# Kernel tuning notes

Hardware: AMD Instinct MI355X
Metric: run time of the kernel (lower is better)

The kernel has to match this reference:

```python
import jax, jax.numpy as jnp
import numpy as np

S, B, C, H, W = 3, 4, 256, 64, 64
NH, HD = 8, 32  # heads, head_dim (C = NH*HD)
EPS = 1e-5  # BatchNorm eps (torch default)


def _bn_params(k, n, c):
    k1, k2, k3, k4 = jax.random.split(k, 4)
    gamma = 1.0 + 0.1 * jax.random.normal(k1, (n, c))
    beta = 0.1 * jax.random.normal(k2, (n, c))
    mean = 0.1 * jax.random.normal(k3, (n, c))
    var = jax.random.uniform(k4, (n, c), minval=0.5, maxval=1.5)
    return jnp.stack([gamma, beta, mean, var], axis=1).astype(jnp.float32)  # [n,4,c]


def setup_inputs() -> dict:
    key = jax.random.key(0)
    ks = jax.random.split(key, 20)
    rn = lambda k, sh, s=0.02: (s * jax.random.normal(k, sh)).astype(jnp.float32)
    inp = {
        'x': jax.random.normal(ks[0], (S, B, C, H, W), jnp.float32),
        'Wq': rn(ks[1], (S, C, C)), 'bq': rn(ks[2], (S, C)), 'bn_q': _bn_params(ks[3], S, C),
        'Wk': rn(ks[4], (S, C, C)), 'bk': rn(ks[5], (S, C)), 'bn_k': _bn_params(ks[6], S, C),
        'Wv': rn(ks[7], (S, C, C)), 'bv': rn(ks[8], (S, C)), 'bn_v': _bn_params(ks[9], S, C),
        'imp_w1': rn(ks[10], (C, S * C)), 'imp_b1': rn(ks[10], (C,)),
        'imp_w2': rn(ks[11], (S, C)), 'imp_b2': rn(ks[11], (S,)),
        'attn_in_w': rn(ks[12], (3 * C, C)), 'attn_in_b': rn(ks[13], (3 * C,)),
        'attn_out_w': rn(ks[14], (C, C)), 'attn_out_b': rn(ks[15], (C,)),
        'op_w1': rn(ks[16], (C, C, 3, 3)), 'op_b1': rn(ks[17], (C,)),
        'op_bn': _bn_params(ks[18], 1, C)[0],  # [4,C]
        'op_w2': rn(ks[19], (C, C)), 'op_b2': rn(ks[19], (C,)),
        'target_h': H, 'target_w': W,
    }
    return inp


def _proj(x, Wt, bt, bnt):
    # per-scale 1x1 conv + BatchNorm (inference) + exact GELU; x:[S,B,C,H,W]
    y = jnp.einsum('sbchw,soc->sbohw', x, Wt) + bt[:, None, :, None, None]
    g, be, mu, var = bnt[:, 0], bnt[:, 1], bnt[:, 2], bnt[:, 3]
    sc = g * jax.lax.rsqrt(var + EPS)
    y = (y - mu[:, None, :, None, None]) * sc[:, None, :, None, None] + be[:, None, :, None, None]
    return jax.nn.gelu(y, approximate=False)


def _bn1(y, bn):  # y:[B,C,H,W], bn:[4,C]
    g, be, mu, var = bn[0], bn[1], bn[2], bn[3]
    sc = g * jax.lax.rsqrt(var + EPS)
    return (y - mu[None, :, None, None]) * sc[None, :, None, None] + be[None, :, None, None]


def _forward(x, Wq, bq, bn_q, Wk, bk, bn_k, Wv, bv, bn_v,
             imp_w1, imp_b1, imp_w2, imp_b2,
             attn_in_w, attn_in_b, attn_out_w, attn_out_b,
             op_w1, op_b1, op_bn, op_w2, op_b2):
    # scale-importance weights from global pooled concat [B, S*C]
    pooled = x.mean(axis=(3, 4)).transpose(1, 0, 2).reshape(B, S * C)
    h = jax.nn.gelu(pooled @ imp_w1.T + imp_b1, approximate=False)
    w = jax.nn.softmax(h @ imp_w2.T + imp_b2, axis=1)  # [B,S]

    q = _proj(x, Wq, bq, bn_q)
    k = _proj(x, Wk, bk, bn_k)
    v = _proj(x, Wv, bv, bn_v)

    N = B * H * W
    tok = lambda t: t.transpose(1, 3, 4, 0, 2).reshape(N, S, C)  # [N,S,C]
    Wiq, Wik, Wiv = attn_in_w[:C], attn_in_w[C:2 * C], attn_in_w[2 * C:]
    biq, bik, biv = attn_in_b[:C], attn_in_b[C:2 * C], attn_in_b[2 * C:]
    qt = (tok(q) @ Wiq.T + biq).reshape(N, S, NH, HD).transpose(0, 2, 1, 3)
    kt = (tok(k) @ Wik.T + bik).reshape(N, S, NH, HD).transpose(0, 2, 1, 3)
    vt = (tok(v) @ Wiv.T + biv).reshape(N, S, NH, HD).transpose(0, 2, 1, 3)
    scores = jnp.einsum('nhsd,nhtd->nhst', qt, kt) / jnp.sqrt(jnp.float32(HD))
    attn = jax.nn.softmax(scores, axis=-1)  # dropout=0.1 is inactive in eval
    o = jnp.einsum('nhst,nhtd->nhsd', attn, vt).transpose(0, 2, 1, 3).reshape(N, S, C)
    o = o @ attn_out_w.T + attn_out_b
    attn_sp = o.reshape(B, H, W, S, C).transpose(3, 0, 4, 1, 2)  # [S,B,C,H,W]

    integrated = jnp.einsum('sbchw,bs->bchw', attn_sp, w)

    y = jax.lax.conv_general_dilated(integrated, op_w1, (1, 1), 'SAME',
                                     dimension_numbers=('NCHW', 'OIHW', 'NCHW'))
    y = y + op_b1[None, :, None, None]
    y = jax.nn.gelu(_bn1(y, op_bn), approximate=False)
    y = jnp.einsum('bchw,oc->bohw', y, op_w2) + op_b2[None, :, None, None]
    return y + x[1]  # residual with second (resized) scale


def reference(x, Wq, bq, bn_q, Wk, bk, bn_k, Wv, bv, bn_v,
              imp_w1, imp_b1, imp_w2, imp_b2,
              attn_in_w, attn_in_b, attn_out_w, attn_out_b,
              op_w1, op_b1, op_bn, op_w2, op_b2, target_h, target_w):
    return _forward(x, Wq, bq, bn_q, Wk, bk, bn_k, Wv, bv, bn_v,
                    imp_w1, imp_b1, imp_w2, imp_b2,
                    attn_in_w, attn_in_b, attn_out_w, attn_out_b,
                    op_w1, op_b1, op_bn, op_w2, op_b2)
```

## Files before the change

### kernel.cpp

```cpp
#include <hip/hip_runtime.h>
#include <hip/hip_bf16.h>
#include <math.h>

#define S_ 3
#define B_ 4
#define C_ 256
#define H_ 64
#define W_ 64
#define HW_ 4096
#define CHW_ (C_*HW_)
#define NH_ 8
#define HD_ 32
#define EPS_ 1e-5f

typedef float  f32x4 __attribute__((ext_vector_type(4)));
typedef short  s16x8 __attribute__((ext_vector_type(8)));
typedef unsigned short u16x4 __attribute__((ext_vector_type(4)));
typedef unsigned int   u32x2 __attribute__((ext_vector_type(2)));
typedef int    s32x4 __attribute__((ext_vector_type(4)));

static constexpr size_t HALFB  = (size_t)S_*B_*CHW_*2;
static constexpr size_t QB     = (size_t)B_*CHW_*2;
static constexpr size_t O_XB   = 0;
static constexpr size_t O_S0B  = HALFB;
static constexpr size_t O_BUFA = 2*HALFB;
static constexpr size_t O_BUFB = 3*HALFB;
static constexpr size_t O_OMB  = 4*HALFB;
static constexpr size_t O_INTB = 4*HALFB + QB;
static constexpr size_t O_CVB  = 4*HALFB + 2*QB;
static constexpr size_t O_AW   = 4*HALFB + 3*QB;
static constexpr size_t O_WB   = O_AW + (size_t)B_*NH_*3*HW_*4;
static constexpr size_t WB_ELEMS = 1507328;
static constexpr size_t O_POOL = O_WB + WB_ELEMS*2;
static constexpr size_t O_H    = O_POOL + (size_t)B_*S_*C_*4;
static constexpr size_t O_WSM  = O_H + (size_t)B_*C_*4;
static constexpr size_t WO_WQ  = 0;
static constexpr size_t WO_WK  = 196608;
static constexpr size_t WO_WV  = 393216;
static constexpr size_t WO_AIW = 589824;
static constexpr size_t WO_AOW = 786432;
static constexpr size_t WO_CW  = 851968;
static constexpr size_t WO_FW2 = 1441792;

__device__ __forceinline__ float gelu_exact(float x) {
    return 0.5f * x * (1.0f + erff(x * 0.70710678118654752440f));
}
__device__ __forceinline__ unsigned short f2bf(float f) {
    union { float f; unsigned u; } x; x.f = f;
    unsigned r = x.u + 0x7FFFu + ((x.u >> 16) & 1u);
    return (unsigned short)(r >> 16);
}
__device__ __forceinline__ float bf2f(unsigned short h) {
    union { unsigned u; float f; } x; x.u = ((unsigned)h) << 16;
    return x.f;
}

__global__ __launch_bounds__(256)
void cast_w(const float* __restrict__ w0, const float* __restrict__ w1,
            const float* __restrict__ w2, const float* __restrict__ w3,
            const float* __restrict__ w4, const float* __restrict__ w5,
            const float* __restrict__ w6, unsigned short* __restrict__ dst) {
    int blk = blockIdx.x;
    const float* src; size_t base;
    if      (blk < 48)  { src = w0; base = WO_WQ;  }
    else if (blk < 96)  { src = w1; base = WO_WK;  blk -= 48; }
    else if (blk < 144) { src = w2; base = WO_WV;  blk -= 96; }
    else if (blk < 192) { src = w3; base = WO_AIW; blk -= 144; }
    else if (blk < 208) { src = w4; base = WO_AOW; blk -= 192; }
    else if (blk < 352) { src = w5; base = WO_CW;  blk -= 208; }
    else                { src = w6; base = WO_FW2; blk -= 352; }
    size_t off = (size_t)blk*4096 + threadIdx.x*4;
    #pragma unroll
    for (int it = 0; it < 4; ++it, off += 1024) {
        float4 v = *(const float4*)&src[off];
        u16x4 h; h[0] = f2bf(v.x); h[1] = f2bf(v.y); h[2] = f2bf(v.z); h[3] = f2bf(v.w);
        *(u16x4*)&dst[base + off] = h;
    }
}

__global__ __launch_bounds__(256)
void cast_pool(const float* __restrict__ x, unsigned short* __restrict__ xb,
               float* __restrict__ pooled) {
    const int blk = blockIdx.x;
    const int c  = blk & (C_-1);
    const int sb = blk >> 8;
    const int s  = sb >> 2, b = sb & 3;
    const float* p = x + (size_t)blk * HW_;
    unsigned short* q = xb + (size_t)blk * HW_;
    float sum = 0.f;
    int i = threadIdx.x * 4;
    #pragma unroll
    for (int it = 0; it < 4; ++it, i += 1024) {
        float4 v = *(const float4*)&p[i];
        sum += v.x + v.y + v.z + v.w;
        u16x4 h; h[0] = f2bf(v.x); h[1] = f2bf(v.y); h[2] = f2bf(v.z); h[3] = f2bf(v.w);
        *(u16x4*)&q[i] = h;
    }
    #pragma unroll
    for (int off = 32; off; off >>= 1) sum += __shfl_down(sum, off);
    __shared__ float red[4];
    if ((threadIdx.x & 63) == 0) red[threadIdx.x >> 6] = sum;
    __syncthreads();
    if (threadIdx.x == 0) {
        float t = red[0] + red[1] + red[2] + red[3];
        pooled[b * (S_*C_) + s * C_ + c] = t * (1.0f / HW_);
    }
}

__global__ __launch_bounds__(256)
void imp1(const float* __restrict__ pooled, const float* __restrict__ w1,
          const float* __restrict__ b1, float* __restrict__ h) {
    const int o = blockIdx.x;
    const int tid = threadIdx.x;
    float part[4] = {0.f, 0.f, 0.f, 0.f};
    for (int j = tid; j < S_*C_; j += 256) {
        const float wv = w1[o * (S_*C_) + j];
        #pragma unroll
        for (int b = 0; b < 4; ++b) part[b] = fmaf(pooled[b*(S_*C_) + j], wv, part[b]);
    }
    #pragma unroll
    for (int off = 32; off; off >>= 1)
        #pragma unroll
        for (int b = 0; b < 4; ++b) part[b] += __shfl_down(part[b], off);
    __shared__ float red[4][4];
    if ((tid & 63) == 0) {
        #pragma unroll
        for (int b = 0; b < 4; ++b) red[tid >> 6][b] = part[b];
    }
    __syncthreads();
    if (tid < 4) {
        float t = red[0][tid] + red[1][tid] + red[2][tid] + red[3][tid];
        h[tid * C_ + o] = gelu_exact(t + b1[o]);
    }
}

__global__ __launch_bounds__(256)
void imp2(const float* __restrict__ h, const float* __restrict__ w2,
          const float* __restrict__ b2, float* __restrict__ wout) {
    __shared__ float hl[B_*C_];
    __shared__ float lg[4][3];
    const int tid = threadIdx.x;
    for (int i = tid; i < B_*C_; i += 256) hl[i] = h[i];
    __syncthreads();
    if (tid < 12) {
        const int b = tid / 3, s = tid % 3;
        float a = b2[s];
        for (int o = 0; o < C_; ++o) a = fmaf(hl[b*C_ + o], w2[s*C_ + o], a);
        lg[b][s] = a;
    }
    __syncthreads();
    if (tid < 4) {
        const float m = fmaxf(fmaxf(lg[tid][0], lg[tid][1]), lg[tid][2]);
        const float e0 = expf(lg[tid][0]-m), e1 = expf(lg[tid][1]-m), e2 = expf(lg[tid][2]-m);
        const float inv = 1.0f / (e0 + e1 + e2);
        wout[tid*3+0] = e0*inv; wout[tid*3+1] = e1*inv; wout[tid*3+2] = e2*inv;
    }
}

template<int MODE>
__global__ __launch_bounds__(256)
void mgemm(const unsigned short* __restrict__ In, const unsigned short* __restrict__ Wb,
           const float* __restrict__ bias, const float* __restrict__ bnp,
           const float* __restrict__ resid, void* __restrict__ Out, int perS) {
    __shared__ __align__(16) unsigned short Ash[4096];
    __shared__ __align__(16) unsigned short Bsh[4096];
    __shared__ float2 ep[128];

    const int z    = blockIdx.z;
    const int widx = perS ? (z >> 2) : 0;
    const unsigned short* Wm = Wb + (size_t)widx * (C_*C_);
    const unsigned short* in = In + (size_t)z * CHW_;
    const int tid  = threadIdx.x;
    const int lane = tid & 63;
    const int wid  = tid >> 6;
    const int nBase = blockIdx.x * 128;
    const int mBase = blockIdx.y * 128;
    const int wm = (wid >> 1) * 64;
    const int wn = (wid & 1) * 64;

    if (tid < 128) {
        const int o = mBase + tid;
        float mulc = 1.f, addc = bias[widx*C_ + o];
        if constexpr (MODE == 0) {
            const float g  = bnp[(size_t)widx*4*C_ + o];
            const float be = bnp[(size_t)widx*4*C_ + C_   + o];
            const float mu = bnp[(size_t)widx*4*C_ + 2*C_ + o];
            const float va = bnp[(size_t)widx*4*C_ + 3*C_ + o];
            mulc = g * rsqrtf(va + EPS_);
            addc = (addc - mu) * mulc + be;
        }
        ep[tid] = make_float2(mulc, addc);
    }

    const f32x4 zero = {0.f, 0.f, 0.f, 0.f};
    f32x4 acc[4][4];
    #pragma unroll
    for (int i = 0; i < 4; ++i)
        #pragma unroll
        for (int j = 0; j < 4; ++j) acc[i][j] = zero;

    for (int k0 = 0; k0 < C_; k0 += 32) {
        __syncthreads();
        #pragma unroll
        for (int it = 0; it < 4; ++it) {
            const int idx = tid + it*256;
            const int m = idx >> 3, q = idx & 7;
            u16x4 v = *(const u16x4*)&Wm[(size_t)(mBase + m)*C_ + k0 + 4*q];
            u32x2 w; w[0] = (unsigned)v[0] | ((unsigned)v[1] << 16);
                     w[1] = (unsigned)v[2] | ((unsigned)v[3] << 16);
            *(u32x2*)((char*)Ash + ((m>>4)*1024 + ((m&15) + 16*(q>>1))*16 + (q&1)*8)) = w;
        }
        #pragma unroll
        for (int it = 0; it < 4; ++it) {
            const int idx = tid + it*256;
            const int n = idx & 127, kq = idx >> 7;
            const size_t gb = (size_t)(k0 + 4*kq)*HW_ + nBase + n;
            unsigned short e0 = in[gb], e1 = in[gb + HW_], e2 = in[gb + 2*HW_], e3 = in[gb + 3*HW_];
            u32x2 w; w[0] = (unsigned)e0 | ((unsigned)e1 << 16);
                     w[1] = (unsigned)e2 | ((unsigned)e3 << 16);
            *(u32x2*)((char*)Bsh + ((n>>4)*1024 + ((n&15) + 16*(kq>>1))*16 + (kq&1)*8)) = w;
        }
        __syncthreads();
        s16x8 af[4], bfv[4];
        #pragma unroll
        for (int mi = 0; mi < 4; ++mi)
            af[mi] = *(const s16x8*)((const char*)Ash + (((wm>>4) + mi)*1024 + lane*16));
        #pragma unroll
        for (int ni = 0; ni < 4; ++ni)
            bfv[ni] = *(const s16x8*)((const char*)Bsh + (((wn>>4) + ni)*1024 + lane*16));
        #pragma unroll
        for (int mi = 0; mi < 4; ++mi)
            #pragma unroll
            for (int ni = 0; ni < 4; ++ni)
                acc[mi][ni] = __builtin_amdgcn_mfma_f32_16x16x32_bf16(af[mi], bfv[ni], acc[mi][ni], 0, 0, 0);
    }

    const int cb = wn + (lane & 15);
    const int r0 = (lane >> 4) * 4;
    if constexpr (MODE == 2) {
        float* out = (float*)Out + (size_t)z * CHW_;
        const float* rs = resid + (size_t)z * CHW_;
        #pragma unroll
        for (int mi = 0; mi < 4; ++mi)
            #pragma unroll
            for (int j = 0; j < 4; ++j) {
                const int ro = wm + mi*16 + r0 + j;
                const float2 ma = ep[ro];
                const size_t row = (size_t)(mBase + ro)*HW_ + nBase;
                #pragma unroll
                for (int ni = 0; ni < 4; ++ni) {
                    const int n = cb + ni*16;
                    out[row + n] = fmaf(acc[mi][ni][j], ma.x, ma.y) + rs[row + n];
                }
            }
    } else {
        unsigned short* out = (unsigned short*)Out + (size_t)z * CHW_;
        #pragma unroll
        for (int mi = 0; mi < 4; ++mi)
            #pragma unroll
            for (int j = 0; j < 4; ++j) {
                const int ro = wm + mi*16 + r0 + j;
                const float2 ma = ep[ro];
                const size_t row = (size_t)(mBase + ro)*HW_ + nBase;
                #pragma unroll
                for (int ni = 0; ni < 4; ++ni) {
                    const int n = cb + ni*16;
                    float v = fmaf(acc[mi][ni][j], ma.x, ma.y);
                    if constexpr (MODE == 0) v = gelu_exact(v);
                    out[row + n] = f2bf(v);
                }
            }
    }
}

__global__ __launch_bounds__(256)
void conv_mfma(const unsigned short* __restrict__ In, const unsigned short* __restrict__ Wc,
               const float* __restrict__ bias, const float* __restrict__ bnp,
               unsigned short* __restrict__ Out) {
    __shared__ __align__(16) int T[9*C_];
    __shared__ __align__(16) unsigned short Ash[4096];
    __shared__ __align__(16) unsigned short Bsh[2048];
    __shared__ float2 ep[128];

    const int b = blockIdx.z;
    const unsigned short* in = In + (size_t)b * CHW_;
    const int tid  = threadIdx.x;
    const int lane = tid & 63;
    const int wid  = tid >> 6;
    const int yrow  = blockIdx.x;
    const int mBase = blockIdx.y * 128;
    const int wm = (wid >> 1) * 64;
    const int wn = (wid & 1) * 32;

    for (int kk = tid; kk < 9*C_; kk += 256) {
        const int c   = kk / 9;
        const int tap = kk - 9*c;
        const int t3  = tap / 3;
        const int dx  = tap - t3*3 - 1;
        const int off = c*HW_ + (t3 - 1)*W_ + dx;
        T[kk] = (t3 << 22) | ((dx + 1) << 20) | (off + 65);
    }
    if (tid < 128) {
        const int o = mBase + tid;
        const float g  = bnp[o];
        const float be = bnp[C_   + o];
        const float mu = bnp[2*C_ + o];
        const float va = bnp[3*C_ + o];
        const float mulc = g * rsqrtf(va + EPS_);
        ep[tid] = make_float2(mulc, (bias[o] - mu) * mulc + be);
    }

    const f32x4 zero = {0.f, 0.f, 0.f, 0.f};
    f32x4 acc[4][2];
    #pragma unroll
    for (int i = 0; i < 4; ++i) { acc[i][0] = zero; acc[i][1] = zero; }

    const int base2 = yrow*W_;

    for (int k0 = 0; k0 < 9*C_; k0 += 32) {
        __syncthreads();
        #pragma unroll
        for (int it = 0; it < 4; ++it) {
            const int idx = tid + it*256;
            const int m = idx >> 3, q = idx & 7;
            u16x4 v = *(const u16x4*)&Wc[(size_t)(mBase + m)*(9*C_) + k0 + 4*q];
            u32x2 w; w[0] = (unsigned)v[0] | ((unsigned)v[1] << 16);
                     w[1] = (unsigned)v[2] | ((unsigned)v[3] << 16);
            *(u32x2*)((char*)Ash + ((m>>4)*1024 + ((m&15) + 16*(q>>1))*16 + (q&1)*8)) = w;
        }
        #pragma unroll
        for (int it = 0; it < 2; ++it) {
            const int idx = tid + it*256;
            const int n = idx & 63, kq = idx >> 6;
            s32x4 tv = *(const s32x4*)&T[k0 + 4*kq];
            unsigned short e[4];
            #pragma unroll
            for (int j = 0; j < 4; ++j) {
                const int v  = tv[j];
                const int sy = yrow + ((v >> 22) & 3) - 1;
                const int sx = n    + ((v >> 20) & 3) - 1;
                const int off = (v & 0xFFFFF) - 65;
                e[j] = ((unsigned)sy < (unsigned)H_ && (unsigned)sx < (unsigned)W_)
                       ? in[off + base2 + n] : (unsigned short)0;
            }
            u32x2 w; w[0] = (unsigned)e[0] | ((unsigned)e[1] << 16);
                     w[1] = (unsigned)e[2] | ((unsigned)e[3] << 16);
            *(u32x2*)((char*)Bsh + ((n>>4)*1024 + ((n&15) + 16*(kq>>1))*16 + (kq&1)*8)) = w;
        }
        __syncthreads();
        s16x8 af[4], bfv[2];
        #pragma unroll
        for (int mi = 0; mi < 4; ++mi)
            af[mi] = *(const s16x8*)((const char*)Ash + (((wm>>4) + mi)*1024 + lane*16));
        #pragma unroll
        for (int ni = 0; ni < 2; ++ni)
            bfv[ni] = *(const s16x8*)((const char*)Bsh + (((wn>>4) + ni)*1024 + lane*16));
        #pragma unroll
        for (int mi = 0; mi < 4; ++mi)
            #pragma unroll
            for (int ni = 0; ni < 2; ++ni)
                acc[mi][ni] = __builtin_amdgcn_mfma_f32_16x16x32_bf16(af[mi], bfv[ni], acc[mi][ni], 0, 0, 0);
    }

    unsigned short* out = Out + (size_t)b * CHW_;
    const int cb = wn + (lane & 15);
    const int r0 = (lane >> 4) * 4;
    #pragma unroll
    for (int mi = 0; mi < 4; ++mi)
        #pragma unroll
        for (int j = 0; j < 4; ++j) {
            const int ro = wm + mi*16 + r0 + j;
            const float2 ma = ep[ro];
            const size_t row = (size_t)(mBase + ro)*HW_ + yrow*W_;
            #pragma unroll
            for (int ni = 0; ni < 2; ++ni) {
                const int n = cb + ni*16;
                out[row + n] = f2bf(gelu_exact(fmaf(acc[mi][ni][j], ma.x, ma.y)));
            }
        }
}

__global__ __launch_bounds__(256)
void attn_scores(const unsigned short* __restrict__ QT, const unsigned short* __restrict__ KT,
                 const float* __restrict__ wsm, float* __restrict__ AW) {
    const int gid = blockIdx.x * 256 + threadIdx.x;
    const int b  = gid >> 12;
    const int hw = gid & (HW_-1);
    const float w0 = wsm[b*3+0], w1 = wsm[b*3+1], w2 = wsm[b*3+2];
    const size_t sStride = (size_t)B_ * CHW_;
    for (int h = 0; h < NH_; ++h) {
        const size_t base = ((size_t)b*C_ + h*HD_)*HW_ + hw;
        float s00=0,s01=0,s02=0,s10=0,s11=0,s12=0,s20=0,s21=0,s22=0;
        #pragma unroll 8
        for (int d = 0; d < HD_; ++d) {
            const size_t off = base + (size_t)d*HW_;
            const float q0 = bf2f(QT[off]), q1 = bf2f(QT[off+sStride]), q2 = bf2f(QT[off+2*sStride]);
            const float k0 = bf2f(KT[off]), k1 = bf2f(KT[off+sStride]), k2 = bf2f(KT[off+2*sStride]);
            s00 = fmaf(q0,k0,s00); s01 = fmaf(q0,k1,s01); s02 = fmaf(q0,k2,s02);
            s10 = fmaf(q1,k0,s10); s11 = fmaf(q1,k1,s11); s12 = fmaf(q1,k2,s12);
            s20 = fmaf(q2,k0,s20); s21 = fmaf(q2,k1,s21); s22 = fmaf(q2,k2,s22);
        }
        const float scl = 0.17677669529663687f;
        float aw0[3], aw1[3], aw2[3];
        {
            float m = fmaxf(fmaxf(s00,s01),s02);
            float e0 = expf(s00*scl - m*scl), e1 = expf(s01*scl - m*scl), e2 = expf(s02*scl - m*scl);
            float inv = 1.f/(e0+e1+e2); aw0[0]=e0*inv; aw0[1]=e1*inv; aw0[2]=e2*inv;
        }
        {
            float m = fmaxf(fmaxf(s10,s11),s12);
            float e0 = expf(s10*scl - m*scl), e1 = expf(s11*scl - m*scl), e2 = expf(s12*scl - m*scl);
            float inv = 1.f/(e0+e1+e2); aw1[0]=e0*inv; aw1[1]=e1*inv; aw1[2]=e2*inv;
        }
        {
            float m = fmaxf(fmaxf(s20,s21),s22);
            float e0 = expf(s20*scl - m*scl), e1 = expf(s21*scl - m*scl), e2 = expf(s22*scl - m*scl);
            float inv = 1.f/(e0+e1+e2); aw2[0]=e0*inv; aw2[1]=e1*inv; aw2[2]=e2*inv;
        }
        #pragma unroll
        for (int t = 0; t < 3; ++t) {
            const float a = w0*aw0[t] + w1*aw1[t] + w2*aw2[t];
            AW[(((size_t)b*NH_ + h)*3 + t)*HW_ + hw] = a;
        }
    }
}

__global__ __launch_bounds__(256)
void om_combine(const unsigned short* __restrict__ VT, const float* __restrict__ AW,
                unsigned short* __restrict__ OM) {
    const int gid = blockIdx.x * 256 + threadIdx.x;
    const int hw = gid & (HW_-1);
    const int c  = (gid >> 12) & (C_-1);
    const int b  = gid >> 20;
    const int h  = c >> 5;
    float r = 0.f;
    #pragma unroll
    for (int t = 0; t < 3; ++t)
        r = fmaf(AW[(((size_t)b*NH_ + h)*3 + t)*HW_ + hw],
                 bf2f(VT[((size_t)(t*B_ + b)*C_ + c)*HW_ + hw]), r);
    OM[gid] = f2bf(r);
}

extern "C" void kernel_launch(void* const* d_in, const int* in_sizes, int n_in,
                              void* d_out, int out_size, void* d_ws, size_t ws_size,
                              hipStream_t stream) {
    (void)in_sizes; (void)n_in; (void)out_size; (void)ws_size;
    const float* x   = (const float*)d_in[0];
    const float* Wq  = (const float*)d_in[1];
    const float* bq  = (const float*)d_in[2];
    const float* bnq = (const float*)d_in[3];
    const float* Wk  = (const float*)d_in[4];
    const float* bk  = (const float*)d_in[5];
    const float* bnk = (const float*)d_in[6];
    const float* Wv  = (const float*)d_in[7];
    const float* bv  = (const float*)d_in[8];
    const float* bnv = (const float*)d_in[9];
    const float* iw1 = (const float*)d_in[10];
    const float* ib1 = (const float*)d_in[11];
    const float* iw2 = (const float*)d_in[12];
    const float* ib2 = (const float*)d_in[13];
    const float* aiw = (const float*)d_in[14];
    const float* aib = (const float*)d_in[15];
    const float* aow = (const float*)d_in[16];
    const float* aob = (const float*)d_in[17];
    const float* cw  = (const float*)d_in[18];
    const float* cb  = (const float*)d_in[19];
    const float* cbn = (const float*)d_in[20];
    const float* fw2 = (const float*)d_in[21];
    const float* fb2 = (const float*)d_in[22];

    char* wsb = (char*)d_ws;
    unsigned short* xb   = (unsigned short*)(wsb + O_XB);
    unsigned short* s0b  = (unsigned short*)(wsb + O_S0B);
    unsigned short* bufA = (unsigned short*)(wsb + O_BUFA);
    unsigned short* bufB = (unsigned short*)(wsb + O_BUFB);
    unsigned short* OMb  = (unsigned short*)(wsb + O_OMB);
    unsigned short* INTb = (unsigned short*)(wsb + O_INTB);
    unsigned short* CVb  = (unsigned short*)(wsb + O_CVB);
    float* aw_buf        = (float*)(wsb + O_AW);
    unsigned short* WB   = (unsigned short*)(wsb + O_WB);
    float* pooled        = (float*)(wsb + O_POOL);
    float* hbuf          = (float*)(wsb + O_H);
    float* wsm           = (float*)(wsb + O_WSM);
    float* out           = (float*)d_out;

    const unsigned short* Wqb  = WB + WO_WQ;
    const unsigned short* Wkb  = WB + WO_WK;
    const unsigned short* Wvb  = WB + WO_WV;
    const unsigned short* aiwb = WB + WO_AIW;
    const unsigned short* aowb = WB + WO_AOW;
    const unsigned short* cwb  = WB + WO_CW;
    const unsigned short* fw2b = WB + WO_FW2;

    cast_w<<<dim3(368), 256, 0, stream>>>(Wq, Wk, Wv, aiw, aow, cw, fw2, WB);
    cast_pool<<<dim3(S_*B_*C_), 256, 0, stream>>>(x, xb, pooled);
    imp1<<<dim3(C_), 256, 0, stream>>>(pooled, iw1, ib1, hbuf);
    imp2<<<dim3(1), 256, 0, stream>>>(hbuf, iw2, ib2, wsm);

    const dim3 g12(HW_/128, C_/128, S_*B_);
    const dim3 g4 (HW_/128, C_/128, B_);
    const dim3 gc (H_, C_/128, B_);

    mgemm<0><<<g12, 256, 0, stream>>>(xb, Wqb, bq, bnq, nullptr, s0b, 1);
    mgemm<1><<<g12, 256, 0, stream>>>(s0b, aiwb, aib, nullptr, nullptr, bufA, 0);
    mgemm<0><<<g12, 256, 0, stream>>>(xb, Wkb, bk, bnk, nullptr, s0b, 1);
    mgemm<1><<<g12, 256, 0, stream>>>(s0b, aiwb + C_*C_, aib + C_, nullptr, nullptr, bufB, 0);
    attn_scores<<<dim3(B_*HW_/256), 256, 0, stream>>>(bufA, bufB, wsm, aw_buf);
    mgemm<0><<<g12, 256, 0, stream>>>(xb, Wvb, bv, bnv, nullptr, s0b, 1);
    mgemm<1><<<g12, 256, 0, stream>>>(s0b, aiwb + 2*C_*C_, aib + 2*C_, nullptr, nullptr, bufA, 0);
    om_combine<<<dim3(B_*CHW_/256), 256, 0, stream>>>(bufA, aw_buf, OMb);
    mgemm<1><<<g4, 256, 0, stream>>>(OMb, aowb, aob, nullptr, nullptr, INTb, 0);
    conv_mfma<<<gc, 256, 0, stream>>>(INTb, cwb, cb, cbn, CVb);
    mgemm<2><<<g4, 256, 0, stream>>>(CVb, fw2b, fb2, nullptr, x + (size_t)B_*CHW_, out, 0);
}
```

Before: 452.2 us.

## Register-prefetch K=64 tiles in GEMM and conv, reorder conv weights tap-major

The GEMM and 3x3 conv kernels now load the next K=64 slice into registers while the MFMAs run on the current one, which halves the number of barrier pairs per K. Global reads go straight into an MFMA-ready shared-memory layout with 16-byte stores. The conv weights are recast tap-major in a new cast kernel, so each 64-wide K chunk shares one tap, and the per-block lookup table of tap offsets is removed. The cost is doubled shared memory and extra prefetch registers, which may lower occupancy.

After: 413.1 us. 1.09x faster.

```diff
diff --git a/kernel.cpp b/kernel.cpp
--- a/kernel.cpp
+++ b/kernel.cpp
@@ -12,12 +12,11 @@
 #define NH_ 8
 #define HD_ 32
 #define EPS_ 1e-5f
+#define K9_ (9*C_)
 
 typedef float  f32x4 __attribute__((ext_vector_type(4)));
 typedef short  s16x8 __attribute__((ext_vector_type(8)));
 typedef unsigned short u16x4 __attribute__((ext_vector_type(4)));
-typedef unsigned int   u32x2 __attribute__((ext_vector_type(2)));
-typedef int    s32x4 __attribute__((ext_vector_type(4)));
 
 static constexpr size_t HALFB  = (size_t)S_*B_*CHW_*2;
 static constexpr size_t QB     = (size_t)B_*CHW_*2;
@@ -59,7 +58,7 @@
 void cast_w(const float* __restrict__ w0, const float* __restrict__ w1,
             const float* __restrict__ w2, const float* __restrict__ w3,
             const float* __restrict__ w4, const float* __restrict__ w5,
-            const float* __restrict__ w6, unsigned short* __restrict__ dst) {
+            unsigned short* __restrict__ dst) {
     int blk = blockIdx.x;
     const float* src; size_t base;
     if      (blk < 48)  { src = w0; base = WO_WQ;  }
@@ -67,8 +66,7 @@
     else if (blk < 144) { src = w2; base = WO_WV;  blk -= 96; }
     else if (blk < 192) { src = w3; base = WO_AIW; blk -= 144; }
     else if (blk < 208) { src = w4; base = WO_AOW; blk -= 192; }
-    else if (blk < 352) { src = w5; base = WO_CW;  blk -= 208; }
-    else                { src = w6; base = WO_FW2; blk -= 352; }
+    else                { src = w5; base = WO_FW2; blk -= 208; }
     size_t off = (size_t)blk*4096 + threadIdx.x*4;
     #pragma unroll
     for (int it = 0; it < 4; ++it, off += 1024) {
@@ -76,6 +74,15 @@
         u16x4 h; h[0] = f2bf(v.x); h[1] = f2bf(v.y); h[2] = f2bf(v.z); h[3] = f2bf(v.w);
         *(u16x4*)&dst[base + off] = h;
     }
+}
+
+__global__ __launch_bounds__(256)
+void cast_cw(const float* __restrict__ src, unsigned short* __restrict__ dst) {
+    const int o = blockIdx.x;
+    const int c = threadIdx.x;
+    #pragma unroll
+    for (int tap = 0; tap < 9; ++tap)
+        dst[(size_t)o*K9_ + tap*C_ + c] = f2bf(src[(size_t)o*K9_ + c*9 + tap]);
 }
 
 __global__ __launch_bounds__(256)
@@ -162,8 +169,8 @@
 void mgemm(const unsigned short* __restrict__ In, const unsigned short* __restrict__ Wb,
            const float* __restrict__ bias, const float* __restrict__ bnp,
            const float* __restrict__ resid, void* __restrict__ Out, int perS) {
-    __shared__ __align__(16) unsigned short Ash[4096];
-    __shared__ __align__(16) unsigned short Bsh[4096];
+    __shared__ __align__(16) unsigned short Ash[8192];
+    __shared__ __align__(16) unsigned short Bsh[8192];
     __shared__ float2 ep[128];
 
     const int z    = blockIdx.z;
@@ -192,6 +199,30 @@
         ep[tid] = make_float2(mulc, addc);
     }
 
+    s16x8 ar[4], br[4];
+    auto LOADA = [&](int k0) {
+        #pragma unroll
+        for (int it = 0; it < 4; ++it) {
+            const int idx = tid + it*256;
+            const int h = idx >> 9, r = idx & 511;
+            const int m = ((r >> 6) << 4) + (r & 15), p = (r & 63) >> 4;
+            ar[it] = *(const s16x8*)&Wm[(size_t)(mBase + m)*C_ + k0 + h*32 + 8*p];
+        }
+    };
+    auto LOADB = [&](int k0) {
+        #pragma unroll
+        for (int it = 0; it < 4; ++it) {
+            const int idx = tid + it*256;
+            const int h = idx >> 9, r = idx & 511;
+            const int n = ((r >> 6) << 4) + (r & 15), p = (r & 63) >> 4;
+            const size_t gb = (size_t)(k0 + h*32 + 8*p)*HW_ + nBase + n;
+            s16x8 v;
+            #pragma unroll
+            for (int j = 0; j < 8; ++j) v[j] = (short)in[gb + (size_t)j*HW_];
+            br[it] = v;
+        }
+    };
+
     const f32x4 zero = {0.f, 0.f, 0.f, 0.f};
     f32x4 acc[4][4];
     #pragma unroll
@@ -199,40 +230,31 @@
         #pragma unroll
         for (int j = 0; j < 4; ++j) acc[i][j] = zero;
 
-    for (int k0 = 0; k0 < C_; k0 += 32) {
+    LOADA(0); LOADB(0);
+    for (int k0 = 0; k0 < C_; k0 += 64) {
+        #pragma unroll
+        for (int it = 0; it < 4; ++it) {
+            *(s16x8*)((char*)Ash + (tid + it*256)*16) = ar[it];
+            *(s16x8*)((char*)Bsh + (tid + it*256)*16) = br[it];
+        }
         __syncthreads();
-        #pragma unroll
-        for (int it = 0; it < 4; ++it) {
-            const int idx = tid + it*256;
-            const int m = idx >> 3, q = idx & 7;
-            u16x4 v = *(const u16x4*)&Wm[(size_t)(mBase + m)*C_ + k0 + 4*q];
-            u32x2 w; w[0] = (unsigned)v[0] | ((unsigned)v[1] << 16);
-                     w[1] = (unsigned)v[2] | ((unsigned)v[3] << 16);
-            *(u32x2*)((char*)Ash + ((m>>4)*1024 + ((m&15) + 16*(q>>1))*16 + (q&1)*8)) = w;
-        }
-        #pragma unroll
-        for (int it = 0; it < 4; ++it) {
-            const int idx = tid + it*256;
-            const int n = idx & 127, kq = idx >> 7;
-            const size_t gb = (size_t)(k0 + 4*kq)*HW_ + nBase + n;
-            unsigned short e0 = in[gb], e1 = in[gb + HW_], e2 = in[gb + 2*HW_], e3 = in[gb + 3*HW_];
-            u32x2 w; w[0] = (unsigned)e0 | ((unsigned)e1 << 16);
-                     w[1] = (unsigned)e2 | ((unsigned)e3 << 16);
-            *(u32x2*)((char*)Bsh + ((n>>4)*1024 + ((n&15) + 16*(kq>>1))*16 + (kq&1)*8)) = w;
+        if (k0 + 64 < C_) { LOADA(k0 + 64); LOADB(k0 + 64); }
+        #pragma unroll
+        for (int h = 0; h < 2; ++h) {
+            s16x8 af[4], bfv[4];
+            #pragma unroll
+            for (int mi = 0; mi < 4; ++mi)
+                af[mi] = *(const s16x8*)((const char*)Ash + h*8192 + ((wm>>4) + mi)*1024 + lane*16);
+            #pragma unroll
+            for (int ni = 0; ni < 4; ++ni)
+                bfv[ni] = *(const s16x8*)((const char*)Bsh + h*8192 + ((wn>>4) + ni)*1024 + lane*16);
+            #pragma unroll
+            for (int mi = 0; mi < 4; ++mi)
+                #pragma unroll
+                for (int ni = 0; ni < 4; ++ni)
+                    acc[mi][ni] = __builtin_amdgcn_mfma_f32_16x16x32_bf16(af[mi], bfv[ni], acc[mi][ni], 0, 0, 0);
         }
         __syncthreads();
-        s16x8 af[4], bfv[4];
-        #pragma unroll
-        for (int mi = 0; mi < 4; ++mi)
-            af[mi] = *(const s16x8*)((const char*)Ash + (((wm>>4) + mi)*1024 + lane*16));
-        #pragma unroll
-        for (int ni = 0; ni < 4; ++ni)
-            bfv[ni] = *(const s16x8*)((const char*)Bsh + (((wn>>4) + ni)*1024 + lane*16));
-        #pragma unroll
-        for (int mi = 0; mi < 4; ++mi)
-            #pragma unroll
-            for (int ni = 0; ni < 4; ++ni)
-                acc[mi][ni] = __builtin_amdgcn_mfma_f32_16x16x32_bf16(af[mi], bfv[ni], acc[mi][ni], 0, 0, 0);
     }
 
     const int cb = wn + (lane & 15);
@@ -277,9 +299,8 @@
 void conv_mfma(const unsigned short* __restrict__ In, const unsigned short* __restrict__ Wc,
                const float* __restrict__ bias, const float* __restrict__ bnp,
                unsigned short* __restrict__ Out) {
-    __shared__ __align__(16) int T[9*C_];
-    __shared__ __align__(16) unsigned short Ash[4096];
-    __shared__ __align__(16) unsigned short Bsh[2048];
+    __shared__ __align__(16) unsigned short Ash[8192];
+    __shared__ __align__(16) unsigned short Bsh[4096];
     __shared__ float2 ep[128];
 
     const int b = blockIdx.z;
@@ -292,14 +313,6 @@
     const int wm = (wid >> 1) * 64;
     const int wn = (wid & 1) * 32;
 
-    for (int kk = tid; kk < 9*C_; kk += 256) {
-        const int c   = kk / 9;
-        const int tap = kk - 9*c;
-        const int t3  = tap / 3;
-        const int dx  = tap - t3*3 - 1;
-        const int off = c*HW_ + (t3 - 1)*W_ + dx;
-        T[kk] = (t3 << 22) | ((dx + 1) << 20) | (off + 65);
-    }
     if (tid < 128) {
         const int o = mBase + tid;
         const float g  = bnp[o];
@@ -310,56 +323,71 @@
         ep[tid] = make_float2(mulc, (bias[o] - mu) * mulc + be);
     }
 
+    s16x8 ar[4], br[2];
+    auto LOADA = [&](int k0) {
+        #pragma unroll
+        for (int it = 0; it < 4; ++it) {
+            const int idx = tid + it*256;
+            const int h = idx >> 9, r = idx & 511;
+            const int m = ((r >> 6) << 4) + (r & 15), p = (r & 63) >> 4;
+            ar[it] = *(const s16x8*)&Wc[(size_t)(mBase + m)*K9_ + k0 + h*32 + 8*p];
+        }
+    };
+    auto LOADB = [&](int k0) {
+        const int tap = k0 >> 8;
+        const int c0  = k0 & 255;
+        const int t3  = tap / 3;
+        const int dy  = t3 - 1;
+        const int dx  = tap - t3*3 - 1;
+        const int sy  = yrow + dy;
+        const bool rowOK = (unsigned)sy < (unsigned)H_;
+        #pragma unroll
+        for (int it = 0; it < 2; ++it) {
+            const int idx = tid + it*256;
+            const int h = idx >> 8, r = idx & 255;
+            const int n = ((r >> 6) << 4) + (r & 15), p = (r & 63) >> 4;
+            const int sx = n + dx;
+            s16x8 v = {0,0,0,0,0,0,0,0};
+            if (rowOK && (unsigned)sx < (unsigned)W_) {
+                const size_t gb = (size_t)(c0 + h*32 + 8*p)*HW_ + sy*W_ + sx;
+                #pragma unroll
+                for (int j = 0; j < 8; ++j) v[j] = (short)in[gb + (size_t)j*HW_];
+            }
+            br[it] = v;
+        }
+    };
+
     const f32x4 zero = {0.f, 0.f, 0.f, 0.f};
     f32x4 acc[4][2];
     #pragma unroll
     for (int i = 0; i < 4; ++i) { acc[i][0] = zero; acc[i][1] = zero; }
 
-    const int base2 = yrow*W_;
-
-    for (int k0 = 0; k0 < 9*C_; k0 += 32) {
+    LOADA(0); LOADB(0);
+    for (int k0 = 0; k0 < K9_; k0 += 64) {
+        #pragma unroll
+        for (int it = 0; it < 4; ++it)
+            *(s16x8*)((char*)Ash + (tid + it*256)*16) = ar[it];
+        #pragma unroll
+        for (int it = 0; it < 2; ++it)
+            *(s16x8*)((char*)Bsh + (tid + it*256)*16) = br[it];
         __syncthreads();
-        #pragma unroll
-        for (int it = 0; it < 4; ++it) {
-            const int idx = tid + it*256;
-            const int m = idx >> 3, q = idx & 7;
-            u16x4 v = *(const u16x4*)&Wc[(size_t)(mBase + m)*(9*C_) + k0 + 4*q];
-            u32x2 w; w[0] = (unsigned)v[0] | ((unsigned)v[1] << 16);
-                     w[1] = (unsigned)v[2] | ((unsigned)v[3] << 16);
-            *(u32x2*)((char*)Ash + ((m>>4)*1024 + ((m&15) + 16*(q>>1))*16 + (q&1)*8)) = w;
-        }
-        #pragma unroll
-        for (int it = 0; it < 2; ++it) {
-            const int idx = tid + it*256;
-            const int n = idx & 63, kq = idx >> 6;
-            s32x4 tv = *(const s32x4*)&T[k0 + 4*kq];
-            unsigned short e[4];
-            #pragma unroll
-            for (int j = 0; j < 4; ++j) {
-                const int v  = tv[j];
-                const int sy = yrow + ((v >> 22) & 3) - 1;
-                const int sx = n    + ((v >> 20) & 3) - 1;
-                const int off = (v & 0xFFFFF) - 65;
-                e[j] = ((unsigned)sy < (unsigned)H_ && (unsigned)sx < (unsigned)W_)
-                       ? in[off + base2 + n] : (unsigned short)0;
-            }
-            u32x2 w; w[0] = (unsigned)e[0] | ((unsigned)e[1] << 16);
-                     w[1] = (unsigned)e[2] | ((unsigned)e[3] << 16);
-            *(u32x2*)((char*)Bsh + ((n>>4)*1024 + ((n&15) + 16*(kq>>1))*16 + (kq&1)*8)) = w;
+        if (k0 + 64 < K9_) { LOADA(k0 + 64); LOADB(k0 + 64); }
+        #pragma unroll
+        for (int h = 0; h < 2; ++h) {
+            s16x8 af[4], bfv[2];
+            #pragma unroll
+            for (int mi = 0; mi < 4; ++mi)
+                af[mi] = *(const s16x8*)((const char*)Ash + h*8192 + ((wm>>4) + mi)*1024 + lane*16);
+            #pragma unroll
+            for (int ni = 0; ni < 2; ++ni)
+                bfv[ni] = *(const s16x8*)((const char*)Bsh + h*4096 + ((wn>>4) + ni)*1024 + lane*16);
+            #pragma unroll
+            for (int mi = 0; mi < 4; ++mi)
+                #pragma unroll
+                for (int ni = 0; ni < 2; ++ni)
+                    acc[mi][ni] = __builtin_amdgcn_mfma_f32_16x16x32_bf16(af[mi], bfv[ni], acc[mi][ni], 0, 0, 0);
         }
         __syncthreads();
-        s16x8 af[4], bfv[2];
-        #pragma unroll
-        for (int mi = 0; mi < 4; ++mi)
-            af[mi] = *(const s16x8*)((const char*)Ash + (((wm>>4) + mi)*1024 + lane*16));
-        #pragma unroll
-        for (int ni = 0; ni < 2; ++ni)
-            bfv[ni] = *(const s16x8*)((const char*)Bsh + (((wn>>4) + ni)*1024 + lane*16));
-        #pragma unroll
-        for (int mi = 0; mi < 4; ++mi)
-            #pragma unroll
-            for (int ni = 0; ni < 2; ++ni)
-                acc[mi][ni] = __builtin_amdgcn_mfma_f32_16x16x32_bf16(af[mi], bfv[ni], acc[mi][ni], 0, 0, 0);
     }
 
     unsigned short* out = Out + (size_t)b * CHW_;
@@ -492,7 +520,8 @@
     const unsigned short* cwb  = WB + WO_CW;
     const unsigned short* fw2b = WB + WO_FW2;
 
-    cast_w<<<dim3(368), 256, 0, stream>>>(Wq, Wk, Wv, aiw, aow, cw, fw2, WB);
+    cast_w<<<dim3(224), 256, 0, stream>>>(Wq, Wk, Wv, aiw, aow, fw2, WB);
+    cast_cw<<<dim3(256), 256, 0, stream>>>(cw, (unsigned short*)(WB + WO_CW));
     cast_pool<<<dim3(S_*B_*C_), 256, 0, stream>>>(x, xb, pooled);
     imp1<<<dim3(C_), 256, 0, stream>>>(pooled, iw1, ib1, hbuf);
     imp2<<<dim3(1), 256, 0, stream>>>(hbuf, iw2, ib2, wsm);
```
